# Kernel tuning notes

Measured on AMD Instinct MI355X. Metric: run time of the kernel, lower is better.

## Reference

```python
import jax, jax.numpy as jnp
import numpy as np

NUM_HEADS = 16
NUM_KV_HEADS = 4
ROPE_THETA = 10000.0


def apply_rope(x, position_ids, theta):
    # x: [B, S, h, d]; position_ids: [B, S]
    d = x.shape[-1]
    freqs = 1.0 / theta ** (jnp.arange(0, d, 2, dtype=jnp.float32) / d)  # [d/2]
    angles = position_ids.astype(jnp.float32)[..., None] * freqs          # [B, S, d/2]
    cos = jnp.cos(angles)[:, :, None, :]                                  # [B, S, 1, d/2]
    sin = jnp.sin(angles)[:, :, None, :]
    xr = x.astype(jnp.float32).reshape(*x.shape[:-1], d // 2, 2)
    x0, x1 = xr[..., 0], xr[..., 1]
    o0 = x0 * cos - x1 * sin
    o1 = x0 * sin + x1 * cos
    out = jnp.stack((o0, o1), axis=-1).reshape(*x.shape)
    return out.astype(x.dtype)


def setup_inputs() -> dict:
    key = jax.random.key(0)
    k0, k1, k2, k3, k4 = jax.random.split(key, 5)
    B, S, H = 1, 2048, 2048
    Hkv = H // (NUM_HEADS // NUM_KV_HEADS)  # 512
    init_scale = 0.02 / np.sqrt(H)
    return {
        "hidden_states": jax.random.normal(k0, (B, S, H), jnp.float32),
        "attention_mask": jnp.ones((B, S), jnp.int32),
        "segment_ids": jnp.zeros((B, S), jnp.int32),
        "position_ids": jnp.broadcast_to(jnp.arange(S, dtype=jnp.int32)[None], (B, S)),
        "Wq": jax.random.normal(k1, (H, H), jnp.float32) * init_scale,
        "Wk": jax.random.normal(k2, (H, Hkv), jnp.float32) * init_scale,
        "Wv": jax.random.normal(k3, (H, Hkv), jnp.float32) * init_scale,
        "Wo": jax.random.normal(k4, (H, H), jnp.float32) * init_scale,
    }


def reference(hidden_states, attention_mask, segment_ids, position_ids, Wq, Wk, Wv, Wo):
    B, S, H = hidden_states.shape
    nh, nkv = NUM_HEADS, NUM_KV_HEADS
    g = nh // nkv
    hd = H // nh

    xq = (hidden_states @ Wq).reshape(B, S, nh, hd)
    xk = (hidden_states @ Wk).reshape(B, S, nkv, hd)
    xv = (hidden_states @ Wv).reshape(B, S, nkv, hd)
    # GQA repeat: 'b s (h d) -> b s (h g) d' == repeat each kv head g times contiguously
    xk = jnp.repeat(xk, g, axis=2)  # [B, S, nh, hd]
    xv = jnp.repeat(xv, g, axis=2)

    xq = apply_rope(xq, position_ids, ROPE_THETA)
    xk = apply_rope(xk, position_ids, ROPE_THETA)

    # masks: causal AND padding AND segment
    causal = jnp.tril(jnp.ones((S, S), dtype=bool))[None, None]            # [1,1,S,S]
    pad = (attention_mask > 0)[:, None, None, :]                            # [B,1,1,S]
    seg = (segment_ids[:, :, None] == segment_ids[:, None, :])[:, None]     # [B,1,S,S]
    mask = causal & pad & seg                                               # [B,1,S,S]

    scale = 1.0 / np.sqrt(hd)
    logits = jnp.einsum("bqhd,bkhd->bhqk", xq.astype(jnp.float32), xk.astype(jnp.float32)) * scale
    logits = jnp.where(mask, logits, jnp.finfo(jnp.float32).min)
    probs = jax.nn.softmax(logits, axis=-1).astype(xv.dtype)
    attn = jnp.einsum("bhqk,bkhd->bqhd", probs, xv)                         # [B,S,nh,hd]

    out = attn.reshape(B, S, H) @ Wo
    return out
```

## Files before the change

### kernel.cpp

```cpp
#include <hip/hip_runtime.h>
#include <hip/hip_bf16.h>
#include <stdint.h>
#include <math.h>

#define SS 2048
#define HH 2048
#define NH 16
#define NKV 4
#define HD 128
#define HKV 512
#define NQKV 3072

typedef __bf16 bf16x8 __attribute__((ext_vector_type(8)));
typedef float f32x4 __attribute__((ext_vector_type(4)));

static_assert(sizeof(bf16x8) == 16, "bf16x8 must be 16B");

__device__ __forceinline__ void async_ld16(const void* gp, void* lp) {
  __builtin_amdgcn_global_load_lds(
      (const __attribute__((address_space(1))) unsigned int*)(uintptr_t)gp,
      (__attribute__((address_space(3))) unsigned int*)(uintptr_t)lp,
      16, 0, 0);
}

__device__ __forceinline__ unsigned short f2bu(float f) {
  __hip_bfloat16 b = __float2bfloat16(f);
  return *reinterpret_cast<unsigned short*>(&b);
}

__global__ __launch_bounds__(256) void k_prep1(
    const float* __restrict__ X, const float* __restrict__ Wq, const float* __restrict__ Wk,
    const float* __restrict__ Wv, const float* __restrict__ Wo,
    const int* __restrict__ amv, const int* __restrict__ seg, int* __restrict__ kseg,
    float2* __restrict__ rtab,
    __hip_bfloat16* __restrict__ Xb, __hip_bfloat16* __restrict__ WqT,
    __hip_bfloat16* __restrict__ WkT, __hip_bfloat16* __restrict__ WvT,
    __hip_bfloat16* __restrict__ WoT) {
  __shared__ __align__(16) __hip_bfloat16 t2[64 * 72];
  int b = blockIdx.x;
  int t = threadIdx.y * 32 + threadIdx.x;
  if (b < 4096) {
    int i = b * 256 + t;
    float4 v = ((const float4*)X)[i];
    ushort4 o;
    o.x = f2bu(v.x); o.y = f2bu(v.y); o.z = f2bu(v.z); o.w = f2bu(v.w);
    ((ushort4*)Xb)[i] = o;
    return;
  }
  b -= 4096;
  if (b >= 2568) {
    int i = (b - 2568) * 256 + t;
    int p = i >> 6, f = i & 63;
    const float L2T_D64 = 0.20762050593046837f;
    float freq = exp2f(-L2T_D64 * (float)f);
    float sn, cs;
    sincosf((float)p * freq, &sn, &cs);
    rtab[i] = make_float2(sn, cs);
    return;
  }
  if (b >= 2560) {
    int i = (b - 2560) * 256 + t;
    kseg[i] = (amv[i] > 0) ? seg[i] : 0x7fffffff;
    return;
  }
  const float* src; __hip_bfloat16* dst; int xtiles;
  if (b < 1024)      { src = Wq; dst = WqT; xtiles = 32; }
  else if (b < 2048) { src = Wo; dst = WoT; xtiles = 32; b -= 1024; }
  else if (b < 2304) { src = Wk; dst = WkT; xtiles = 8;  b -= 2048; }
  else               { src = Wv; dst = WvT; xtiles = 8;  b -= 2304; }
  const int C = xtiles * 64;
  int bx = (b % xtiles) * 64;
  int by = (b / xtiles) * 64;
#pragma unroll
  for (int i = 0; i < 4; i++) {
    int idx = i * 256 + t;
    int r = idx >> 4, c4 = (idx & 15) * 4;
    float4 v = *(const float4*)(src + (size_t)(by + r) * C + bx + c4);
    t2[(c4 + 0) * 72 + r] = __float2bfloat16(v.x);
    t2[(c4 + 1) * 72 + r] = __float2bfloat16(v.y);
    t2[(c4 + 2) * 72 + r] = __float2bfloat16(v.z);
    t2[(c4 + 3) * 72 + r] = __float2bfloat16(v.w);
  }
  __syncthreads();
#pragma unroll
  for (int i = 0; i < 2; i++) {
    int idx = i * 256 + t;
    int rr = idx >> 3, cc = (idx & 7) * 8;
    *(bf16x8*)(dst + (size_t)(bx + rr) * HH + by + cc) =
        *(const bf16x8*)(&t2[rr * 72 + cc]);
  }
}

__global__ __launch_bounds__(256, 2) void k_gemm_qkv(
    const __hip_bfloat16* __restrict__ A, const __hip_bfloat16* __restrict__ B,
    __hip_bfloat16* __restrict__ Qb, __hip_bfloat16* __restrict__ Kb,
    __hip_bfloat16* __restrict__ Vt, const int* __restrict__ pos,
    const float2* __restrict__ rtab) {
  __shared__ __align__(16) __hip_bfloat16 sA[2][128 * 64];
  __shared__ __align__(16) __hip_bfloat16 sB[2][96 * 64];
  const int tid = threadIdx.x;
  const int lane = tid & 63;
  const int wave = tid >> 6;
  const int lid = blockIdx.x;
  const int swz = (lid & 7) * 64 + (lid >> 3);
  const int bm = (swz >> 5) * 128;
  const int bn = (swz & 31) * 96;
  const int wm = (wave & 1) * 64;
  const int wn = (wave >> 1) * 48;
  const int am = lane & 15;
  const int ch = lane >> 4;

  f32x4 acc[4][3] = {};

  auto stage = [&](int p, int k0) {
#pragma unroll
    for (int q = 0; q < 4; q++) {
      int c = q * 256 + tid;
      int row = c >> 3, kp = c & 7;
      int col = (kp ^ (row & 7)) * 8;
      async_ld16(A + (size_t)(bm + row) * HH + k0 + col, (char*)&sA[p][0] + c * 16);
    }
#pragma unroll
    for (int q = 0; q < 3; q++) {
      int c = q * 256 + tid;
      int row = c >> 3, kp = c & 7;
      int col = (kp ^ (row & 7)) * 8;
      async_ld16(B + (size_t)(bn + row) * HH + k0 + col, (char*)&sB[p][0] + c * 16);
    }
  };
  auto compute = [&](int p) {
#pragma unroll
    for (int kb = 0; kb < 2; kb++) {
      bf16x8 a[4], b[3];
#pragma unroll
      for (int i = 0; i < 4; i++) {
        int row = wm + i * 16 + am;
        a[i] = *(const bf16x8*)(&sA[p][0] + row * 64 + (((kb * 4 + ch) ^ (row & 7)) * 8));
      }
#pragma unroll
      for (int j = 0; j < 3; j++) {
        int row = wn + j * 16 + am;
        b[j] = *(const bf16x8*)(&sB[p][0] + row * 64 + (((kb * 4 + ch) ^ (row & 7)) * 8));
      }
#pragma unroll
      for (int i = 0; i < 4; i++)
#pragma unroll
        for (int j = 0; j < 3; j++)
          acc[i][j] = __builtin_amdgcn_mfma_f32_16x16x32_bf16(a[i], b[j], acc[i][j], 0, 0, 0);
    }
  };

  stage(0, 0);
  int cur = 0;
  for (int t = 0; t < 32; ++t) {
    if (t + 1 < 32) {
      stage(cur ^ 1, (t + 1) * 64);
      asm volatile("s_waitcnt vmcnt(7)" ::: "memory");
    } else {
      asm volatile("s_waitcnt vmcnt(0)" ::: "memory");
    }
    asm volatile("s_barrier" ::: "memory");
    compute(cur);
    asm volatile("s_barrier" ::: "memory");
    cur ^= 1;
  }

  const float SCLQ = 0.08838834764831845f * 1.4426950408889634f;
  const float sgn = (am & 1) ? 1.0f : -1.0f;
  int pint[4][4];
#pragma unroll
  for (int i = 0; i < 4; i++)
#pragma unroll
    for (int r = 0; r < 4; r++)
      pint[i][r] = pos[bm + wm + i * 16 + ch * 4 + r];
#pragma unroll
  for (int j = 0; j < 3; j++) {
    const int colbase = bn + wn + j * 16;
    const int col = colbase + am;
    if (colbase >= HH + HKV) {
      int lc = col - (HH + HKV);
#pragma unroll
      for (int i = 0; i < 4; i++) {
        int row = bm + wm + i * 16 + ch * 4;
        ushort4 o;
        o.x = f2bu(acc[i][j][0]); o.y = f2bu(acc[i][j][1]);
        o.z = f2bu(acc[i][j][2]); o.w = f2bu(acc[i][j][3]);
        *(ushort4*)(Vt + (size_t)lc * SS + row) = o;
      }
    } else {
      const bool isQ = (colbase < HH);
      int lc = isQ ? col : (col - HH);
      int fidx = (lc >> 1) & 63;
#pragma unroll
      for (int i = 0; i < 4; i++)
#pragma unroll
        for (int r = 0; r < 4; r++) {
          float v = acc[i][j][r];
          float px = __shfl_xor(v, 1, 64);
          float2 sc = rtab[pint[i][r] * 64 + fidx];
          float o = v * sc.y + sgn * px * sc.x;
          int row = bm + wm + i * 16 + ch * 4 + r;
          if (isQ) Qb[(size_t)row * HH + col] = __float2bfloat16(o * SCLQ);
          else     Kb[(size_t)row * HKV + lc] = __float2bfloat16(o);
        }
    }
  }
}

__global__ __launch_bounds__(256, 3) void k_gemm_out(
    const __hip_bfloat16* __restrict__ A, const __hip_bfloat16* __restrict__ B,
    float* __restrict__ C) {
  __shared__ __align__(16) __hip_bfloat16 sA0[64 * 64];
  __shared__ __align__(16) __hip_bfloat16 sB0[128 * 64];
  __shared__ __align__(16) __hip_bfloat16 sA1[64 * 64];
  __shared__ __align__(16) __hip_bfloat16 sB1[128 * 64];
  const int tid = threadIdx.x;
  const int lane = tid & 63;
  const int wave = tid >> 6;
  const int bm = blockIdx.y * 64;
  const int bn = blockIdx.x * 128;
  const int wm = (wave & 1) * 32;
  const int wn = (wave >> 1) * 64;
  const int am = lane & 15;
  const int ch = lane >> 4;

  f32x4 acc[2][4] = {};

  auto stage = [&](__hip_bfloat16* sA, __hip_bfloat16* sB, int k0) {
#pragma unroll
    for (int q = 0; q < 2; q++) {
      int c = q * 256 + tid;
      int row = c >> 3, kp = c & 7;
      int col = (kp ^ (row & 7)) * 8;
      async_ld16(A + (size_t)(bm + row) * HH + k0 + col, (char*)sA + c * 16);
    }
#pragma unroll
    for (int q = 0; q < 4; q++) {
      int c = q * 256 + tid;
      int row = c >> 3, kp = c & 7;
      int col = (kp ^ (row & 7)) * 8;
      async_ld16(B + (size_t)(bn + row) * HH + k0 + col, (char*)sB + c * 16);
    }
  };
  auto compute = [&](const __hip_bfloat16* sA, const __hip_bfloat16* sB) {
#pragma unroll
    for (int kb = 0; kb < 2; kb++) {
      bf16x8 a[2], b[4];
#pragma unroll
      for (int i = 0; i < 2; i++) {
        int row = wm + i * 16 + am;
        a[i] = *(const bf16x8*)(sA + row * 64 + (((kb * 4 + ch) ^ (row & 7)) * 8));
      }
#pragma unroll
      for (int j = 0; j < 4; j++) {
        int row = wn + j * 16 + am;
        b[j] = *(const bf16x8*)(sB + row * 64 + (((kb * 4 + ch) ^ (row & 7)) * 8));
      }
#pragma unroll
      for (int i = 0; i < 2; i++)
#pragma unroll
        for (int j = 0; j < 4; j++)
          acc[i][j] = __builtin_amdgcn_mfma_f32_16x16x32_bf16(a[i], b[j], acc[i][j], 0, 0, 0);
    }
  };

  stage(sA0, sB0, 0);
  int k0 = 0;
  while (true) {
    __syncthreads();
    if (k0 + 64 < HH) stage(sA1, sB1, k0 + 64);
    compute(sA0, sB0);
    k0 += 64; if (k0 >= HH) break;
    __syncthreads();
    if (k0 + 64 < HH) stage(sA0, sB0, k0 + 64);
    compute(sA1, sB1);
    k0 += 64; if (k0 >= HH) break;
  }

#pragma unroll
  for (int i = 0; i < 2; i++)
#pragma unroll
    for (int j = 0; j < 4; j++)
#pragma unroll
      for (int r = 0; r < 4; r++) {
        int row = bm + wm + i * 16 + ch * 4 + r;
        int col = bn + wn + j * 16 + am;
        C[(size_t)row * HH + col] = acc[i][j][r];
      }
}

__global__ __launch_bounds__(256, 4) void k_attn(
    const __hip_bfloat16* __restrict__ Qb,
    const __hip_bfloat16* __restrict__ Kb,
    const __hip_bfloat16* __restrict__ Vt,
    const int* __restrict__ seg,
    const int* __restrict__ kseg,
    float* __restrict__ Obuf,
    float* __restrict__ Lbuf) {
  __shared__ __align__(16) __hip_bfloat16 sK[2][32 * 128];
  __shared__ __align__(16) __hip_bfloat16 sV[2][128 * 32];
  __shared__ __align__(16) __hip_bfloat16 sPall[4][16 * 32];

  const int bid = blockIdx.x;
  const int qt = 31 - (bid >> 5);
  const int h = (bid >> 1) & 15;
  const int half = bid & 1;
  const int T = 2 * (qt + 1);
  const int n0 = qt + 1;
  const int kt0 = half ? n0 : 0;
  const int kt1 = half ? T : n0;

  const int kvh = h >> 2;
  const int tid = threadIdx.x, lane = tid & 63, w = tid >> 6;
  const int am = lane & 15, ch = lane >> 4;
  const int qrow0 = qt * 64 + w * 16;
  char* sP = (char*)&sPall[w][0];

  bf16x8 qf[4];
#pragma unroll
  for (int ks = 0; ks < 4; ks++)
    qf[ks] = *(const bf16x8*)(Qb + (size_t)(qrow0 + am) * HH + h * HD + ks * 32 + ch * 8);

  int segq[4];
#pragma unroll
  for (int r = 0; r < 4; r++) segq[r] = seg[qrow0 + ch * 4 + r];
  const int q0 = seg[qrow0];
  const bool quni = __all((segq[0] == q0) && (segq[1] == q0) &&
                          (segq[2] == q0) && (segq[3] == q0));

  f32x4 o_acc[8] = {};
  float l_s[4] = {0.f, 0.f, 0.f, 0.f};

  auto stage = [&](int kt, int p) {
#pragma unroll
    for (int q = 0; q < 2; q++) {
      int c = q * 256 + tid;
      int row = c >> 4, kp = c & 15;
      int col = (kp ^ (row & 15)) * 8;
      async_ld16(Kb + (size_t)(kt * 32 + row) * HKV + kvh * 128 + col, (char*)sK[p] + c * 16);
    }
#pragma unroll
    for (int q = 0; q < 2; q++) {
      int c = q * 256 + tid;
      int row = c >> 2, kp = c & 3;
      int col = (kp ^ ((row >> 1) & 3)) * 8;
      async_ld16(Vt + (size_t)(kvh * 128 + row) * SS + kt * 32 + col, (char*)sV[p] + c * 16);
    }
  };

  stage(kt0, 0);
  for (int kt = kt0; kt < kt1; kt++) {
    const int p = (kt - kt0) & 1;
    const int kbase = kt * 32;
    const bool skip = (kbase > qrow0 + 15);
    __syncthreads();

    int kinfo[2];
    if (!skip) {
#pragma unroll
      for (int jt = 0; jt < 2; jt++) kinfo[jt] = kseg[kbase + jt * 16 + am];
    }
    if (kt + 1 < kt1) stage(kt + 1, p ^ 1);
    if (!skip) {
      f32x4 sacc[2] = {};
      __builtin_amdgcn_s_setprio(1);
#pragma unroll
      for (int ks = 0; ks < 4; ks++)
#pragma unroll
        for (int jt = 0; jt < 2; jt++) {
          bf16x8 kf = *(const bf16x8*)(sK[p] + (jt * 16 + am) * 128 + (((ks * 4 + ch) ^ am) * 8));
          sacc[jt] = __builtin_amdgcn_mfma_f32_16x16x32_bf16(qf[ks], kf, sacc[jt], 0, 0, 0);
        }
      __builtin_amdgcn_s_setprio(0);

      const bool needc = (kbase + 31 > qrow0);
      const bool fast = quni && !needc &&
          __all((kinfo[0] == q0) && (kinfo[1] == q0));

      if (fast) {
#pragma unroll
        for (int jt = 0; jt < 2; jt++)
#pragma unroll
          for (int r = 0; r < 4; r++) {
            float pv = exp2f(sacc[jt][r] - 8.0f);
            l_s[r] += pv;
            int row = ch * 4 + r;
            int chunk = (jt * 2 + (am >> 3)) ^ (row & 3);
            *(__hip_bfloat16*)(sP + row * 64 + chunk * 16 + (am & 7) * 2) =
                __float2bfloat16(pv);
          }
      } else {
#pragma unroll
        for (int jt = 0; jt < 2; jt++) {
          int kk = kbase + jt * 16 + am;
#pragma unroll
          for (int r = 0; r < 4; r++) {
            int qrow = qrow0 + ch * 4 + r;
            bool ok = (kinfo[jt] == segq[r]) && (kk <= qrow);
            float pv = ok ? exp2f(sacc[jt][r] - 8.0f) : 0.0f;
            l_s[r] += pv;
            int row = ch * 4 + r;
            int chunk = (jt * 2 + (am >> 3)) ^ (row & 3);
            *(__hip_bfloat16*)(sP + row * 64 + chunk * 16 + (am & 7) * 2) =
                __float2bfloat16(pv);
          }
        }
      }

      __builtin_amdgcn_s_setprio(1);
      {
        bf16x8 pf = *(const bf16x8*)(sP + am * 64 + ((ch ^ (am & 3)) * 16));
#pragma unroll
        for (int jt = 0; jt < 8; jt++) {
          int vrow = jt * 16 + am;
          bf16x8 vf = *(const bf16x8*)(sV[p] + vrow * 32 + ((ch ^ ((vrow >> 1) & 3)) * 8));
          o_acc[jt] = __builtin_amdgcn_mfma_f32_16x16x32_bf16(pf, vf, o_acc[jt], 0, 0, 0);
        }
      }
      __builtin_amdgcn_s_setprio(0);
    }
  }

#pragma unroll
  for (int off = 1; off < 16; off <<= 1)
#pragma unroll
    for (int r = 0; r < 4; r++) l_s[r] += __shfl_xor(l_s[r], off, 64);
  if (am == 0)
#pragma unroll
    for (int r = 0; r < 4; r++)
      unsafeAtomicAdd(Lbuf + (size_t)(qrow0 + ch * 4 + r) * NH + h, l_s[r]);
#pragma unroll
  for (int jt = 0; jt < 8; jt++)
#pragma unroll
    for (int r = 0; r < 4; r++) {
      int row = qrow0 + ch * 4 + r;
      unsafeAtomicAdd(Obuf + (size_t)row * HH + h * HD + jt * 16 + am, o_acc[jt][r]);
    }
}

__global__ __launch_bounds__(256) void k_norm(
    const float* __restrict__ Obuf, const float* __restrict__ Lbuf,
    __hip_bfloat16* __restrict__ Ab) {
  int i = blockIdx.x * 256 + threadIdx.x;
  int s = i >> 9;
  int hIdx = (i & 511) >> 5;
  float inv = 1.0f / Lbuf[(size_t)s * NH + hIdx];
  float4 v = ((const float4*)Obuf)[i];
  ushort4 o;
  o.x = f2bu(v.x * inv); o.y = f2bu(v.y * inv);
  o.z = f2bu(v.z * inv); o.w = f2bu(v.w * inv);
  ((ushort4*)Ab)[i] = o;
}

extern "C" void kernel_launch(void* const* d_in, const int* in_sizes, int n_in,
                              void* d_out, int out_size, void* d_ws, size_t ws_size,
                              hipStream_t stream) {
  const float* X  = (const float*)d_in[0];
  const int* amv  = (const int*)d_in[1];
  const int* seg  = (const int*)d_in[2];
  const int* pos  = (const int*)d_in[3];
  const float* Wq = (const float*)d_in[4];
  const float* Wk = (const float*)d_in[5];
  const float* Wv = (const float*)d_in[6];
  const float* Wo = (const float*)d_in[7];
  float* out = (float*)d_out;

  char* ws = (char*)d_ws;
  size_t off = 0;
  auto alloc = [&](size_t bytes) { void* p = ws + off; off += (bytes + 255) & ~(size_t)255; return p; };
  __hip_bfloat16* Xb   = (__hip_bfloat16*)alloc((size_t)SS * HH * 2);
  __hip_bfloat16* WqT  = (__hip_bfloat16*)alloc((size_t)HH * HH * 2);
  __hip_bfloat16* WkT  = (__hip_bfloat16*)alloc((size_t)HKV * HH * 2);
  __hip_bfloat16* WvT  = (__hip_bfloat16*)alloc((size_t)HKV * HH * 2);
  __hip_bfloat16* WoT  = (__hip_bfloat16*)alloc((size_t)HH * HH * 2);
  __hip_bfloat16* Qb   = (__hip_bfloat16*)alloc((size_t)SS * HH * 2);
  __hip_bfloat16* Kb   = (__hip_bfloat16*)alloc((size_t)SS * HKV * 2);
  __hip_bfloat16* Vt   = (__hip_bfloat16*)alloc((size_t)HKV * SS * 2);
  __hip_bfloat16* Ab   = (__hip_bfloat16*)alloc((size_t)SS * HH * 2);
  float*          Obuf = (float*)alloc((size_t)SS * HH * 4);
  float*          Lbuf = (float*)alloc((size_t)SS * NH * 4);
  int*            kseg = (int*)alloc((size_t)SS * 4);
  float2*         rtab = (float2*)alloc((size_t)SS * 64 * 8);
  (void)WkT; (void)WvT;

  hipMemsetAsync(Obuf, 0, (size_t)SS * HH * 4 + ((size_t)SS * NH * 4 + 255 & ~(size_t)255), stream);
  k_prep1<<<dim3(7176), dim3(32, 8), 0, stream>>>(X, Wq, Wk, Wv, Wo, amv, seg, kseg, rtab,
                                                  Xb, WqT, WkT, WvT, WoT);
  k_gemm_qkv<<<dim3(512), 256, 0, stream>>>(Xb, WqT, Qb, Kb, Vt, pos, rtab);
  k_attn<<<dim3(1024), 256, 0, stream>>>(Qb, Kb, Vt, seg, kseg, Obuf, Lbuf);
  k_norm<<<dim3(SS * HH / 4 / 256), 256, 0, stream>>>(Obuf, Lbuf, Ab);
  k_gemm_out<<<dim3(HH / 128, SS / 64), 256, 0, stream>>>(Ab, WoT, out);
}
```

Measured before the change: 222.7 us.

## Split attention KV range four ways, single-buffer LDS, raise occupancy

The attention kernel now splits each (query tile, head) KV range into four chunks instead of two, doubling the grid to 2048 blocks. K/V staging drops from double to single buffering, with a synchronous wait and barrier after each tile load. This halves LDS per block so launch bounds can request 8 waves per SIMD. The P-tile swizzle is also changed to reduce LDS bank conflicts. In exchange, copy/compute overlap inside a block is lost, and the extra splits add more atomic partial-sum traffic to Obuf/Lbuf.

```diff
diff --git a/kernel.cpp b/kernel.cpp
--- a/kernel.cpp
+++ b/kernel.cpp
@@ -289,7 +289,7 @@
       }
 }
 
-__global__ __launch_bounds__(256, 4) void k_attn(
+__global__ __launch_bounds__(256, 8) void k_attn(
     const __hip_bfloat16* __restrict__ Qb,
     const __hip_bfloat16* __restrict__ Kb,
     const __hip_bfloat16* __restrict__ Vt,
@@ -297,18 +297,18 @@
     const int* __restrict__ kseg,
     float* __restrict__ Obuf,
     float* __restrict__ Lbuf) {
-  __shared__ __align__(16) __hip_bfloat16 sK[2][32 * 128];
-  __shared__ __align__(16) __hip_bfloat16 sV[2][128 * 32];
+  __shared__ __align__(16) __hip_bfloat16 sK[32 * 128];
+  __shared__ __align__(16) __hip_bfloat16 sV[128 * 32];
   __shared__ __align__(16) __hip_bfloat16 sPall[4][16 * 32];
 
   const int bid = blockIdx.x;
-  const int qt = 31 - (bid >> 5);
-  const int h = (bid >> 1) & 15;
-  const int half = bid & 1;
+  const int qt = 31 - (bid >> 6);
+  const int h = (bid >> 2) & 15;
+  const int qq = bid & 3;
   const int T = 2 * (qt + 1);
-  const int n0 = qt + 1;
-  const int kt0 = half ? n0 : 0;
-  const int kt1 = half ? T : n0;
+  const int kt0 = (T * qq) >> 2;
+  const int kt1 = (T * (qq + 1)) >> 2;
+  if (kt0 >= kt1) return;
 
   const int kvh = h >> 2;
   const int tid = threadIdx.x, lane = tid & 63, w = tid >> 6;
@@ -331,26 +331,24 @@
   f32x4 o_acc[8] = {};
   float l_s[4] = {0.f, 0.f, 0.f, 0.f};
 
-  auto stage = [&](int kt, int p) {
+  auto stage = [&](int kt) {
 #pragma unroll
     for (int q = 0; q < 2; q++) {
       int c = q * 256 + tid;
       int row = c >> 4, kp = c & 15;
       int col = (kp ^ (row & 15)) * 8;
-      async_ld16(Kb + (size_t)(kt * 32 + row) * HKV + kvh * 128 + col, (char*)sK[p] + c * 16);
+      async_ld16(Kb + (size_t)(kt * 32 + row) * HKV + kvh * 128 + col, (char*)sK + c * 16);
     }
 #pragma unroll
     for (int q = 0; q < 2; q++) {
       int c = q * 256 + tid;
       int row = c >> 2, kp = c & 3;
       int col = (kp ^ ((row >> 1) & 3)) * 8;
-      async_ld16(Vt + (size_t)(kvh * 128 + row) * SS + kt * 32 + col, (char*)sV[p] + c * 16);
+      async_ld16(Vt + (size_t)(kvh * 128 + row) * SS + kt * 32 + col, (char*)sV + c * 16);
     }
   };
 
-  stage(kt0, 0);
   for (int kt = kt0; kt < kt1; kt++) {
-    const int p = (kt - kt0) & 1;
     const int kbase = kt * 32;
     const bool skip = (kbase > qrow0 + 15);
     __syncthreads();
@@ -360,7 +358,10 @@
 #pragma unroll
       for (int jt = 0; jt < 2; jt++) kinfo[jt] = kseg[kbase + jt * 16 + am];
     }
-    if (kt + 1 < kt1) stage(kt + 1, p ^ 1);
+    stage(kt);
+    asm volatile("s_waitcnt vmcnt(0)" ::: "memory");
+    asm volatile("s_barrier" ::: "memory");
+
     if (!skip) {
       f32x4 sacc[2] = {};
       __builtin_amdgcn_s_setprio(1);
@@ -368,7 +369,7 @@
       for (int ks = 0; ks < 4; ks++)
 #pragma unroll
         for (int jt = 0; jt < 2; jt++) {
-          bf16x8 kf = *(const bf16x8*)(sK[p] + (jt * 16 + am) * 128 + (((ks * 4 + ch) ^ am) * 8));
+          bf16x8 kf = *(const bf16x8*)(sK + (jt * 16 + am) * 128 + (((ks * 4 + ch) ^ am) * 8));
           sacc[jt] = __builtin_amdgcn_mfma_f32_16x16x32_bf16(qf[ks], kf, sacc[jt], 0, 0, 0);
         }
       __builtin_amdgcn_s_setprio(0);
@@ -385,7 +386,7 @@
             float pv = exp2f(sacc[jt][r] - 8.0f);
             l_s[r] += pv;
             int row = ch * 4 + r;
-            int chunk = (jt * 2 + (am >> 3)) ^ (row & 3);
+            int chunk = (jt * 2 + (am >> 3)) ^ ch;
             *(__hip_bfloat16*)(sP + row * 64 + chunk * 16 + (am & 7) * 2) =
                 __float2bfloat16(pv);
           }
@@ -400,7 +401,7 @@
             float pv = ok ? exp2f(sacc[jt][r] - 8.0f) : 0.0f;
             l_s[r] += pv;
             int row = ch * 4 + r;
-            int chunk = (jt * 2 + (am >> 3)) ^ (row & 3);
+            int chunk = (jt * 2 + (am >> 3)) ^ ch;
             *(__hip_bfloat16*)(sP + row * 64 + chunk * 16 + (am & 7) * 2) =
                 __float2bfloat16(pv);
           }
@@ -409,11 +410,11 @@
 
       __builtin_amdgcn_s_setprio(1);
       {
-        bf16x8 pf = *(const bf16x8*)(sP + am * 64 + ((ch ^ (am & 3)) * 16));
+        bf16x8 pf = *(const bf16x8*)(sP + am * 64 + (((ch ^ ((am >> 2) & 3)) * 16)));
 #pragma unroll
         for (int jt = 0; jt < 8; jt++) {
           int vrow = jt * 16 + am;
-          bf16x8 vf = *(const bf16x8*)(sV[p] + vrow * 32 + ((ch ^ ((vrow >> 1) & 3)) * 8));
+          bf16x8 vf = *(const bf16x8*)(sV + vrow * 32 + ((ch ^ ((vrow >> 1) & 3)) * 8));
           o_acc[jt] = __builtin_amdgcn_mfma_f32_16x16x32_bf16(pf, vf, o_acc[jt], 0, 0, 0);
         }
       }
@@ -487,7 +488,7 @@
   k_prep1<<<dim3(7176), dim3(32, 8), 0, stream>>>(X, Wq, Wk, Wv, Wo, amv, seg, kseg, rtab,
                                                   Xb, WqT, WkT, WvT, WoT);
   k_gemm_qkv<<<dim3(512), 256, 0, stream>>>(Xb, WqT, Qb, Kb, Vt, pos, rtab);
-  k_attn<<<dim3(1024), 256, 0, stream>>>(Qb, Kb, Vt, seg, kseg, Obuf, Lbuf);
+  k_attn<<<dim3(2048), 256, 0, stream>>>(Qb, Kb, Vt, seg, kseg, Obuf, Lbuf);
   k_norm<<<dim3(SS * HH / 4 / 256), 256, 0, stream>>>(Obuf, Lbuf, Ab);
   k_gemm_out<<<dim3(HH / 128, SS / 64), 256, 0, stream>>>(Ab, WoT, out);
 }
```

Result: slower. 359.8 us (+61.5%).
